# Performance work log

Measured on AMD Instinct MI355X. Metric: run time of the kernel, lower is better.

The kernel has to match this reference:

```python
import jax, jax.numpy as jnp
import numpy as np

B, N, NODE_DIM, EMB, T = 16, 256, 5, 128, 4


def _linear_params(key, din, dout):
    kw, kb = jax.random.split(key)
    s = 1.0 / np.sqrt(din)
    w = jax.random.uniform(kw, (din, dout), minval=-s, maxval=s, dtype=jnp.float32)
    b = jax.random.uniform(kb, (dout,), minval=-s, maxval=s, dtype=jnp.float32)
    return w, b


def setup_inputs() -> dict:
    key = jax.random.key(0)
    ks = jax.random.split(key, 10)
    inp = {
        "xv": jax.random.normal(ks[0], (B, N, NODE_DIM), dtype=jnp.float32),
        "Ws": jax.random.uniform(ks[1], (B, N, N), dtype=jnp.float32),
    }
    inp["t1_w"], inp["t1_b"] = _linear_params(ks[2], NODE_DIM, EMB)
    inp["t2_w"], inp["t2_b"] = _linear_params(ks[3], EMB, EMB)
    inp["t3_w"], inp["t3_b"] = _linear_params(ks[4], EMB, EMB)
    inp["t4_w"], inp["t4_b"] = _linear_params(ks[5], 1, EMB)
    inp["t5_w"], inp["t5_b"] = _linear_params(ks[6], 2 * EMB, 1)
    inp["t6_w"], inp["t6_b"] = _linear_params(ks[7], EMB, EMB)
    inp["t7_w"], inp["t7_b"] = _linear_params(ks[8], EMB, EMB)
    inp["layer_w"], inp["layer_b"] = _linear_params(ks[9], EMB, EMB)
    return inp


def reference(xv, Ws, t1_w, t1_b, t2_w, t2_b, t3_w, t3_b, t4_w, t4_b,
              t5_w, t5_b, t6_w, t6_b, t7_w, t7_b, layer_w, layer_b):
    batch, num_nodes = xv.shape[0], xv.shape[1]
    emb = t1_w.shape[1]
    conn = (Ws > 0).astype(xv.dtype)  # [B,N,N]
    # s1 = layer(relu(theta1(xv)))
    s1 = jnp.maximum(xv @ t1_w + t1_b, 0.0) @ layer_w + layer_b  # [B,N,E]
    # s3 = theta3(sum_i relu(theta4(Ws[:,i,j,None])))
    s3_1 = jnp.maximum(Ws[..., None] * t4_w[0] + t4_b, 0.0)  # [B,N,N,E]
    s3 = s3_1.sum(axis=1) @ t3_w + t3_b  # [B,N,E]
    mu = jnp.zeros((batch, num_nodes, emb), dtype=xv.dtype)
    for _ in range(T):
        s2 = jnp.matmul(conn, mu) @ t2_w + t2_b  # [B,N,E]
        mu = jnp.maximum(s1 + s2 + s3, 0.0)
    # global state: theta6 applied to pooled mu, broadcast to all nodes
    global_state = mu.sum(axis=1, keepdims=True) @ t6_w + t6_b  # [B,1,E]
    global_state = jnp.broadcast_to(global_state, mu.shape)  # [B,N,E]
    local_action = mu @ t7_w + t7_b  # [B,N,E]
    out = jnp.maximum(jnp.concatenate([global_state, local_action], axis=2), 0.0)
    return (out @ t5_w + t5_b).squeeze(2)  # [B,N]
```

## Files before the change

### kernel.cpp

```cpp
#include <hip/hip_runtime.h>

#define BATCH 16
#define NN    256
#define E     128
#define NR    (BATCH*NN)
#define ZCAP  8
#define KP    132

typedef float f4 __attribute__((ext_vector_type(4)));
typedef float f2 __attribute__((ext_vector_type(2)));


__global__ __launch_bounds__(1024) void k_p1(
    const float* __restrict__ xv,  const float* __restrict__ Ws,
    const float* __restrict__ t1w, const float* __restrict__ t1b,
    const float* __restrict__ t3w, const float* __restrict__ t3b,
    const float* __restrict__ t4w, const float* __restrict__ t4b,
    const float* __restrict__ lw,  const float* __restrict__ lb,
    float* __restrict__ s13g, int* __restrict__ zcnt)
{
    const int blk = blockIdx.x;
    const int b   = blk >> 4;
    const int bt  = blk & 15;
    const int j0  = bt * 16;
    const int r0  = b*NN + j0;
    const int t   = threadIdx.x;
    const int e   = t & 127;
    const int q   = t >> 7;

    __shared__ __align__(16) float wst[NN][16];
    __shared__ __align__(16) float s3l[16][KP];
    __shared__ __align__(16) float hsl[16][KP];
    __shared__ int lcnt[16];

    const float* wb = Ws + (size_t)b*NN*NN;

    {
        const int i = t >> 2, jq = (t & 3) * 4;
        *(f4*)&wst[i][jq] = *(const f4*)(wb + (size_t)i*NN + j0 + jq);
    }
    {
        float b1 = t1b[e];
        float w0=t1w[e],w1=t1w[E+e],w2=t1w[2*E+e],w3=t1w[3*E+e],w4=t1w[4*E+e];
        #pragma unroll
        for (int rr = 0; rr < 2; ++rr) {
            const float* x = xv + (size_t)(r0 + q*2 + rr)*5;
            hsl[q*2+rr][e] =
                fmaxf(b1 + x[0]*w0+x[1]*w1+x[2]*w2+x[3]*w3+x[4]*w4, 0.f);
        }
    }
    {
        const int w = t >> 6, l = t & 63;
        f4 v = *(const f4*)(wb + (size_t)(j0 + w)*NN + l*4);
        int c = (v.x<=0.f) + (v.y<=0.f) + (v.z<=0.f) + (v.w<=0.f);
        #pragma unroll
        for (int off = 32; off; off >>= 1) c += __shfl_down(c, off, 64);
        if (l == 0) lcnt[w] = c;
    }
    __syncthreads();
    {
        const int jp = 2*q;
        const float a = t4w[e], c = t4b[e];
        float x0 = 0.f, x1 = 0.f;
        const f2* wp = (const f2*)&wst[0][jp];
        #pragma unroll 8
        for (int i = 0; i < NN; ++i) {
            f2 w = wp[i*8];
            x0 += fmaxf(w.x*a + c, 0.f);
            x1 += fmaxf(w.y*a + c, 0.f);
        }
        s3l[jp][e]   = x0;
        s3l[jp+1][e] = x1;
    }
    __syncthreads();
    {
        const int jp = q*2;
        float acc0 = 0.f, acc1 = 0.f;
        #pragma unroll 2
        for (int k0 = 0; k0 < E; k0 += 4) {
            f4 h0 = *(const f4*)&hsl[jp][k0];
            f4 h1 = *(const f4*)&hsl[jp+1][k0];
            f4 s0 = *(const f4*)&s3l[jp][k0];
            f4 s1 = *(const f4*)&s3l[jp+1][k0];
            #pragma unroll
            for (int m = 0; m < 4; ++m) {
                float wl = lw[(k0+m)*E + e], w3 = t3w[(k0+m)*E + e];
                acc0 += h0[m]*wl + s0[m]*w3;
                acc1 += h1[m]*wl + s1[m]*w3;
            }
        }
        float bb2 = lb[e] + t3b[e];
        s13g[(size_t)(r0+jp)*E + e]   = acc0 + bb2;
        s13g[(size_t)(r0+jp+1)*E + e] = acc1 + bb2;
    }
    if (t < 16) zcnt[r0 + t] = lcnt[t];
}

__global__ __launch_bounds__(1024) void k_p2(
    const float* __restrict__ Ws,
    const float* __restrict__ t2w, const float* __restrict__ t2b,
    const float* __restrict__ t5w,
    const float* __restrict__ t6w, const float* __restrict__ t6b,
    const float* __restrict__ s13g, const int* __restrict__ zcnt,
    float* __restrict__ s2b3g, float* __restrict__ gsumG,
    float* __restrict__ zmu4g)
{
    const int b = blockIdx.x;
    const int t = threadIdx.x;
    const int e = t & 127;
    const int q = t >> 7;
    const size_t bb = (size_t)b*NN*E;

    __shared__ __align__(16) float sQA[8][E];
    __shared__ __align__(16) float sQB[8][E];
    __shared__ __align__(16) float dbuf[E], s2bL[E];
    __shared__ float zmuP[ZCAP][E], zmuN[ZCAP][E];
    __shared__ int   zmap[NN];
    __shared__ int   zlist[ZCAP];
    __shared__ int   nzs;
    __shared__ float sg2[2];

    const float* wb = Ws + (size_t)b*NN*NN;

    if (t == 0) nzs = 0;
    if (t < NN) zmap[t] = -1;
    __syncthreads();
    if (t < NN) {
        if (zcnt[b*NN + t] > 0) {
            int s = atomicAdd(&nzs, 1);
            if (s < ZCAP) { zlist[s] = t; zmap[t] = s; }
        }
    }
    __syncthreads();
    const int nz = nzs < ZCAP ? nzs : ZCAP;

    float reg[32];
    #pragma unroll
    for (int j = 0; j < 32; ++j)
        reg[j] = s13g[bb + (size_t)(q*32+j)*E + e];

    float s2b_r  = t2b[e];
    float s2bP_r = s2b_r;

    for (int it = 0; it < 4; ++it) {
        if (nz > 0) {
            if (q == 0) s2bL[e] = s2b_r;
            __syncthreads();
            for (int z = 0; z < nz; ++z) {
                int j = zlist[z];
                float cp = 0.f;
                const float* wr = wb + (size_t)j*NN;
                if (it > 0) {
                    #pragma unroll
                    for (int u = 0; u < 32; ++u) {
                        int i = q*32 + u;
                        if (wr[i] <= 0.f) {
                            int zi = zmap[i];
                            cp += (zi >= 0) ? zmuP[zi][e]
                                            : fmaxf(reg[u] + s2bP_r, 0.f);
                        }
                    }
                }
                sQA[q][e] = cp;
                __syncthreads();
                if (q == 0) {
                    float s = 0.f;
                    #pragma unroll
                    for (int qq = 0; qq < 8; ++qq) s += sQA[qq][e];
                    dbuf[e] = s;
                }
                __syncthreads();
                float cb = 0.f;
                #pragma unroll 2
                for (int k = 0; k < E; k += 4) {
                    f4 d = *(const f4*)&dbuf[k];
                    cb += d.x*t2w[(k+0)*E+e] + d.y*t2w[(k+1)*E+e]
                        + d.z*t2w[(k+2)*E+e] + d.w*t2w[(k+3)*E+e];
                }
                if (q == 0) {
                    float sj = s13g[bb+(size_t)j*E+e];
                    zmuN[z][e] = fmaxf(sj + s2b_r - cb, 0.f);
                }
                __syncthreads();
            }
        }

        float csp = 0.f;
        #pragma unroll
        for (int u = 0; u < 32; ++u) csp += fmaxf(reg[u] + s2b_r, 0.f);
        sQA[q][e] = csp;
        __syncthreads();

        const float* W = (it < 3) ? t2w : t6w;
        float pa = 0.f;
        #pragma unroll
        for (int g4 = 0; g4 < 4; ++g4) {
            const int k0 = q*16 + g4*4;
            f4 c = *(const f4*)&sQA[0][k0];
            #pragma unroll
            for (int qq = 1; qq < 8; ++qq) {
                f4 d = *(const f4*)&sQA[qq][k0];
                c.x += d.x; c.y += d.y; c.z += d.z; c.w += d.w;
            }
            if (nz > 0) {
                for (int z = 0; z < nz; ++z) {
                    int j = zlist[z];
                    #pragma unroll
                    for (int m = 0; m < 4; ++m) {
                        float sj = s13g[bb+(size_t)j*E + k0 + m];
                        c[m] += zmuN[z][k0+m] - fmaxf(sj + s2bL[k0+m], 0.f);
                    }
                }
            }
            pa += c.x*W[(k0+0)*E+e] + c.y*W[(k0+1)*E+e]
                + c.z*W[(k0+2)*E+e] + c.w*W[(k0+3)*E+e];
        }
        sQB[q][e] = pa;
        s2bP_r = s2b_r;
        if (nz > 0 && q == 0)
            for (int z = 0; z < nz; ++z) zmuP[z][e] = zmuN[z][e];
        __syncthreads();

        if (it < 3) {
            float s = t2b[e];
            #pragma unroll
            for (int qq = 0; qq < 8; ++qq) s += sQB[qq][e];
            s2b_r = s;
        }
    }

    if (q == 0) {
        s2b3g[b*E + e] = s2b_r;
        float g = t6b[e];
        #pragma unroll
        for (int qq = 0; qq < 8; ++qq) g += sQB[qq][e];
        float v = fmaxf(g, 0.f) * t5w[e];
        #pragma unroll
        for (int off = 32; off; off >>= 1) v += __shfl_down(v, off, 64);
        if ((t & 63) == 0) sg2[t >> 6] = v;
        for (int z = 0; z < nz; ++z)
            zmu4g[bb + (size_t)zlist[z]*E + e] = zmuP[z][e];
    }
    if (q == 1 && nzs > ZCAP) {
        for (int j = 0; j < NN; ++j) {
            if (zcnt[b*NN + j] > 0 && zmap[j] < 0) {
                float sj = s13g[bb + (size_t)j*E + e];
                zmu4g[bb + (size_t)j*E + e] = fmaxf(sj + s2b_r, 0.f);
            }
        }
    }
    __syncthreads();
    if (t == 0) gsumG[b] = sg2[0] + sg2[1];
}

__global__ __launch_bounds__(1024) void k_p3(
    const float* __restrict__ t5w, const float* __restrict__ t5b,
    const float* __restrict__ t7w, const float* __restrict__ t7b,
    const float* __restrict__ s13g, const int* __restrict__ zcnt,
    const float* __restrict__ s2b3g, const float* __restrict__ gsumG,
    const float* __restrict__ zmu4g,
    float* __restrict__ out)
{
    const int blk = blockIdx.x;
    const int b   = blk >> 4;
    const int bt  = blk & 15;
    const int j0  = bt * 16;
    const int r0  = b*NN + j0;
    const int t   = threadIdx.x;
    const int e   = t & 127;
    const int q   = t >> 7;

    __shared__ __align__(16) float hsl[16][KP];
    __shared__ float sredO[16][2];

    {
        const int jp = 2*q;
        float s2e = s2b3g[b*E + e];
        #pragma unroll
        for (int rr = 0; rr < 2; ++rr) {
            int row = jp + rr;
            float v;
            if (zcnt[r0 + row] > 0)
                v = zmu4g[(size_t)(r0+row)*E + e];
            else
                v = fmaxf(s13g[(size_t)(r0+row)*E + e] + s2e, 0.f);
            hsl[row][e] = v;
        }
    }
    __syncthreads();
    {
        const int jp = 2*q;
        float a0 = 0.f, a1 = 0.f;
        #pragma unroll 2
        for (int k0 = 0; k0 < E; k0 += 4) {
            f4 m0 = *(const f4*)&hsl[jp][k0];
            f4 m1 = *(const f4*)&hsl[jp+1][k0];
            #pragma unroll
            for (int m = 0; m < 4; ++m) {
                float w7 = t7w[(k0+m)*E + e];
                a0 += m0[m]*w7;
                a1 += m1[m]*w7;
            }
        }
        float b7 = t7b[e], w5 = t5w[E+e];
        float v0 = fmaxf(a0 + b7, 0.f) * w5;
        float v1 = fmaxf(a1 + b7, 0.f) * w5;
        #pragma unroll
        for (int off = 32; off; off >>= 1) {
            v0 += __shfl_down(v0, off, 64);
            v1 += __shfl_down(v1, off, 64);
        }
        if ((t & 63) == 0) {
            sredO[jp][e >> 6]   = v0;
            sredO[jp+1][e >> 6] = v1;
        }
    }
    __syncthreads();
    if (t < 16)
        out[r0 + t] = sredO[t][0] + sredO[t][1] + gsumG[b] + t5b[0];
}

extern "C" void kernel_launch(void* const* d_in, const int* in_sizes, int n_in,
                              void* d_out, int out_size, void* d_ws, size_t ws_size,
                              hipStream_t stream) {
    const float* xv  = (const float*)d_in[0];
    const float* Ws  = (const float*)d_in[1];
    const float* t1w = (const float*)d_in[2];  const float* t1b = (const float*)d_in[3];
    const float* t2w = (const float*)d_in[4];  const float* t2b = (const float*)d_in[5];
    const float* t3w = (const float*)d_in[6];  const float* t3b = (const float*)d_in[7];
    const float* t4w = (const float*)d_in[8];  const float* t4b = (const float*)d_in[9];
    const float* t5w = (const float*)d_in[10]; const float* t5b = (const float*)d_in[11];
    const float* t6w = (const float*)d_in[12]; const float* t6b = (const float*)d_in[13];
    const float* t7w = (const float*)d_in[14]; const float* t7b = (const float*)d_in[15];
    const float* lw  = (const float*)d_in[16]; const float* lb  = (const float*)d_in[17];
    float* outp = (float*)d_out;

    float* ws = (float*)d_ws;
    const int RE = NR*E;
    float* s13g  = ws;
    float* zmu4g = ws + RE;
    float* s2b3g = ws + 2*RE;
    float* gsumG = s2b3g + BATCH*E;
    int*   zcnt  = (int*)(gsumG + 64);

    k_p1<<<256, 1024, 0, stream>>>(xv, Ws, t1w, t1b, t3w, t3b, t4w, t4b,
                                   lw, lb, s13g, zcnt);
    k_p2<<<BATCH, 1024, 0, stream>>>(Ws, t2w, t2b, t5w, t6w, t6b,
                                     s13g, zcnt, s2b3g, gsumG, zmu4g);
    k_p3<<<256, 1024, 0, stream>>>(t5w, t5b, t7w, t7b, s13g, zcnt,
                                   s2b3g, gsumG, zmu4g, outp);
}
```

Baseline: 132.6 us.

## Read Ws columns directly for s3 sums and restructure per-wave matvec tiling

In k_p1 the staging of a Ws column tile into shared memory is removed. Each thread now reads four-wide vectors straight from global memory over half of the i range, and a new shared-memory step adds the two half-sums. The s1/s3 matvecs in k_p1 and the t7 matvec in k_p3 now run on only 8 waves, each handling two rows and two output columns per lane. This gives more register reuse of the weight loads but leaves half the block idle during those matvecs. The KP padding is dropped from shared arrays, and k_p3's reduction collapses to one value per row.

```diff
diff --git a/kernel.cpp b/kernel.cpp
--- a/kernel.cpp
+++ b/kernel.cpp
@@ -5,10 +5,8 @@
 #define E     128
 #define NR    (BATCH*NN)
 #define ZCAP  8
-#define KP    132
 
 typedef float f4 __attribute__((ext_vector_type(4)));
-typedef float f2 __attribute__((ext_vector_type(2)));
 
 
 __global__ __launch_bounds__(1024) void k_p1(
@@ -27,18 +25,16 @@
     const int t   = threadIdx.x;
     const int e   = t & 127;
     const int q   = t >> 7;
-
-    __shared__ __align__(16) float wst[NN][16];
-    __shared__ __align__(16) float s3l[16][KP];
-    __shared__ __align__(16) float hsl[16][KP];
+    const int w   = t >> 6;
+    const int l   = t & 63;
+
+    __shared__ __align__(16) float s3p[2][16][E];
+    __shared__ __align__(16) float s3l[16][E];
+    __shared__ __align__(16) float hsl[16][E];
     __shared__ int lcnt[16];
 
     const float* wb = Ws + (size_t)b*NN*NN;
 
-    {
-        const int i = t >> 2, jq = (t & 3) * 4;
-        *(f4*)&wst[i][jq] = *(const f4*)(wb + (size_t)i*NN + j0 + jq);
-    }
     {
         float b1 = t1b[e];
         float w0=t1w[e],w1=t1w[E+e],w2=t1w[2*E+e],w3=t1w[3*E+e],w4=t1w[4*E+e];
@@ -50,48 +46,60 @@
         }
     }
     {
-        const int w = t >> 6, l = t & 63;
         f4 v = *(const f4*)(wb + (size_t)(j0 + w)*NN + l*4);
         int c = (v.x<=0.f) + (v.y<=0.f) + (v.z<=0.f) + (v.w<=0.f);
         #pragma unroll
         for (int off = 32; off; off >>= 1) c += __shfl_down(c, off, 64);
         if (l == 0) lcnt[w] = c;
     }
-    __syncthreads();
-    {
-        const int jp = 2*q;
+    {
+        const int cq = q & 3, ih = q >> 2;
         const float a = t4w[e], c = t4b[e];
-        float x0 = 0.f, x1 = 0.f;
-        const f2* wp = (const f2*)&wst[0][jp];
+        const float* wcol = wb + (size_t)(ih*128)*NN + j0 + cq*4;
+        float x0=0.f, x1=0.f, x2=0.f, x3=0.f;
         #pragma unroll 8
-        for (int i = 0; i < NN; ++i) {
-            f2 w = wp[i*8];
-            x0 += fmaxf(w.x*a + c, 0.f);
-            x1 += fmaxf(w.y*a + c, 0.f);
-        }
-        s3l[jp][e]   = x0;
-        s3l[jp+1][e] = x1;
-    }
-    __syncthreads();
-    {
-        const int jp = q*2;
-        float acc0 = 0.f, acc1 = 0.f;
+        for (int i = 0; i < 128; ++i) {
+            f4 wv = *(const f4*)(wcol + (size_t)i*NN);
+            x0 += fmaxf(wv.x*a + c, 0.f);
+            x1 += fmaxf(wv.y*a + c, 0.f);
+            x2 += fmaxf(wv.z*a + c, 0.f);
+            x3 += fmaxf(wv.w*a + c, 0.f);
+        }
+        s3p[ih][cq*4+0][e] = x0;
+        s3p[ih][cq*4+1][e] = x1;
+        s3p[ih][cq*4+2][e] = x2;
+        s3p[ih][cq*4+3][e] = x3;
+    }
+    __syncthreads();
+    {
+        s3l[2*q][e]   = s3p[0][2*q][e]   + s3p[1][2*q][e];
+        s3l[2*q+1][e] = s3p[0][2*q+1][e] + s3p[1][2*q+1][e];
+    }
+    __syncthreads();
+    if (w < 8) {
+        const int ra = 2*w, rb = 2*w + 1;
+        float a00=0.f, a01=0.f, a10=0.f, a11=0.f;
         #pragma unroll 2
         for (int k0 = 0; k0 < E; k0 += 4) {
-            f4 h0 = *(const f4*)&hsl[jp][k0];
-            f4 h1 = *(const f4*)&hsl[jp+1][k0];
-            f4 s0 = *(const f4*)&s3l[jp][k0];
-            f4 s1 = *(const f4*)&s3l[jp+1][k0];
+            f4 h0 = *(const f4*)&hsl[ra][k0];
+            f4 h1 = *(const f4*)&hsl[rb][k0];
+            f4 s0 = *(const f4*)&s3l[ra][k0];
+            f4 s1 = *(const f4*)&s3l[rb][k0];
             #pragma unroll
             for (int m = 0; m < 4; ++m) {
-                float wl = lw[(k0+m)*E + e], w3 = t3w[(k0+m)*E + e];
-                acc0 += h0[m]*wl + s0[m]*w3;
-                acc1 += h1[m]*wl + s1[m]*w3;
-            }
-        }
-        float bb2 = lb[e] + t3b[e];
-        s13g[(size_t)(r0+jp)*E + e]   = acc0 + bb2;
-        s13g[(size_t)(r0+jp+1)*E + e] = acc1 + bb2;
+                float wlA = lw[(k0+m)*E + l],      w3A = t3w[(k0+m)*E + l];
+                float wlB = lw[(k0+m)*E + l + 64], w3B = t3w[(k0+m)*E + l + 64];
+                a00 += h0[m]*wlA + s0[m]*w3A;
+                a01 += h0[m]*wlB + s0[m]*w3B;
+                a10 += h1[m]*wlA + s1[m]*w3A;
+                a11 += h1[m]*wlB + s1[m]*w3B;
+            }
+        }
+        float bA = lb[l] + t3b[l], bB = lb[l+64] + t3b[l+64];
+        s13g[(size_t)(r0+ra)*E + l]      = a00 + bA;
+        s13g[(size_t)(r0+ra)*E + l + 64] = a01 + bB;
+        s13g[(size_t)(r0+rb)*E + l]      = a10 + bA;
+        s13g[(size_t)(r0+rb)*E + l + 64] = a11 + bB;
     }
     if (t < 16) zcnt[r0 + t] = lcnt[t];
 }
@@ -269,55 +277,57 @@
     const int t   = threadIdx.x;
     const int e   = t & 127;
     const int q   = t >> 7;
-
-    __shared__ __align__(16) float hsl[16][KP];
-    __shared__ float sredO[16][2];
-
-    {
-        const int jp = 2*q;
+    const int w   = t >> 6;
+    const int l   = t & 63;
+
+    __shared__ __align__(16) float mul[16][E];
+    __shared__ float sredO[16];
+
+    {
         float s2e = s2b3g[b*E + e];
         #pragma unroll
         for (int rr = 0; rr < 2; ++rr) {
-            int row = jp + rr;
+            int row = 2*q + rr;
             float v;
             if (zcnt[r0 + row] > 0)
                 v = zmu4g[(size_t)(r0+row)*E + e];
             else
                 v = fmaxf(s13g[(size_t)(r0+row)*E + e] + s2e, 0.f);
-            hsl[row][e] = v;
-        }
-    }
-    __syncthreads();
-    {
-        const int jp = 2*q;
-        float a0 = 0.f, a1 = 0.f;
+            mul[row][e] = v;
+        }
+    }
+    __syncthreads();
+    if (w < 8) {
+        const int ra = 2*w, rb = 2*w + 1;
+        float a00=0.f, a01=0.f, a10=0.f, a11=0.f;
         #pragma unroll 2
         for (int k0 = 0; k0 < E; k0 += 4) {
-            f4 m0 = *(const f4*)&hsl[jp][k0];
-            f4 m1 = *(const f4*)&hsl[jp+1][k0];
+            f4 m0 = *(const f4*)&mul[ra][k0];
+            f4 m1 = *(const f4*)&mul[rb][k0];
             #pragma unroll
             for (int m = 0; m < 4; ++m) {
-                float w7 = t7w[(k0+m)*E + e];
-                a0 += m0[m]*w7;
-                a1 += m1[m]*w7;
-            }
-        }
-        float b7 = t7b[e], w5 = t5w[E+e];
-        float v0 = fmaxf(a0 + b7, 0.f) * w5;
-        float v1 = fmaxf(a1 + b7, 0.f) * w5;
+                float w7A = t7w[(k0+m)*E + l];
+                float w7B = t7w[(k0+m)*E + l + 64];
+                a00 += m0[m]*w7A;
+                a01 += m0[m]*w7B;
+                a10 += m1[m]*w7A;
+                a11 += m1[m]*w7B;
+            }
+        }
+        float b7A = t7b[l],     b7B = t7b[l+64];
+        float w5A = t5w[E+l],   w5B = t5w[E+l+64];
+        float v0 = fmaxf(a00 + b7A, 0.f)*w5A + fmaxf(a01 + b7B, 0.f)*w5B;
+        float v1 = fmaxf(a10 + b7A, 0.f)*w5A + fmaxf(a11 + b7B, 0.f)*w5B;
         #pragma unroll
         for (int off = 32; off; off >>= 1) {
             v0 += __shfl_down(v0, off, 64);
             v1 += __shfl_down(v1, off, 64);
         }
-        if ((t & 63) == 0) {
-            sredO[jp][e >> 6]   = v0;
-            sredO[jp+1][e >> 6] = v1;
-        }
+        if (l == 0) { sredO[ra] = v0; sredO[rb] = v1; }
     }
     __syncthreads();
     if (t < 16)
-        out[r0 + t] = sredO[t][0] + sredO[t][1] + gsumG[b] + t5b[0];
+        out[r0 + t] = sredO[t] + gsumG[b] + t5b[0];
 }
 
 extern "C" void kernel_launch(void* const* d_in, const int* in_sizes, int n_in,
```

Measured after the change: 135.1 us. No clear change (+1.9%).
